# Performance work log

Hardware: AMD Instinct MI355X
Metric: run time of the kernel (lower is better)

The kernel has to match this reference:

```python
import jax, jax.numpy as jnp
import numpy as np

B, S, H = 4, 256, 128
EXP, DEPTH = 2, 2
MAX_LR = 0.01  # max_adaptive_lr


def l2n(x):
    # F.normalize(x, dim=-1), eps=1e-12
    return x / jnp.maximum(jnp.linalg.norm(x, axis=-1, keepdims=True), 1e-12)


def mem_apply(p, x):
    # ResLinear: depth residual MLP blocks (assumed; ResLinear not in snippet)
    h = x
    for (w1, b1, w2, b2) in p:
        h = h + jax.nn.silu(h @ w1 + b1) @ w2 + b2
    return h


def setup_inputs() -> dict:
    key = jax.random.key(0)
    ks = jax.random.split(key, 16)
    s = 0.02
    d = {
        'x': jax.random.normal(ks[0], (B, S, H), jnp.float32),
        'Wq': jax.random.normal(ks[1], (H, H), jnp.float32) * s,
        'Wk': jax.random.normal(ks[2], (H, H), jnp.float32) * s,
        'Wv': jax.random.normal(ks[3], (H, H), jnp.float32) * s,
        'w_lr': jax.random.normal(ks[4], (H, 1), jnp.float32) * s,
        'b_lr': jnp.zeros((1,), jnp.float32),
        'w_fg': jax.random.normal(ks[5], (H, 1), jnp.float32) * s,
        'b_fg': jnp.zeros((1,), jnp.float32),
        'w_mo': jax.random.normal(ks[6], (H, 1), jnp.float32) * s,
        'b_mo': jnp.zeros((1,), jnp.float32),
    }
    for i in range(DEPTH):
        d[f'w1_{i}'] = jax.random.normal(ks[7 + 2 * i], (H, H * EXP), jnp.float32) * s
        d[f'b1_{i}'] = jnp.zeros((H * EXP,), jnp.float32)
        d[f'w2_{i}'] = jax.random.normal(ks[8 + 2 * i], (H * EXP, H), jnp.float32) * s
        d[f'b2_{i}'] = jnp.zeros((H,), jnp.float32)
        d[f'm_w1_{i}'] = jnp.zeros((H, H * EXP), jnp.float32)
        d[f'm_b1_{i}'] = jnp.zeros((H * EXP,), jnp.float32)
        d[f'm_w2_{i}'] = jnp.zeros((H * EXP, H), jnp.float32)
        d[f'm_b2_{i}'] = jnp.zeros((H,), jnp.float32)
    return d


def _forward(x, Wq, Wk, Wv, w_lr, b_lr, w_fg, b_fg, w_mo, b_mo, p0, m0):
    q = l2n(jax.nn.silu(x @ Wq))                       # [B,S,H]
    k = l2n(jax.nn.silu(x @ Wk))
    v = jax.nn.silu(x @ Wv)
    theta = jax.nn.sigmoid(x @ w_lr + b_lr) * MAX_LR   # [B,S,1]
    alpha = jax.nn.sigmoid(x @ w_fg + b_fg)
    eta = jax.nn.sigmoid(x @ w_mo + b_mo)

    # per-batch copies of memory-net params / momentum
    pb = jax.tree.map(lambda a: jnp.broadcast_to(a, (B,) + a.shape), p0)
    mb = jax.tree.map(lambda a: jnp.broadcast_to(a, (B,) + a.shape), m0)

    def bc(s_, ref):  # [B,1] -> [B,1,...,1] to broadcast over batched param
        return s_.reshape((B,) + (1,) * (ref.ndim - 1))

    def loss_fn(p, k1, v1):
        pred = mem_apply(p, k1)            # [H]
        return jnp.mean((pred - v1) ** 2)  # mse.mean(-1).sum() for 1 token

    def step(carry, inp):
        cp, cm = carry
        kt, vt, qt, th, al, et = inp
        grads = jax.vmap(jax.grad(loss_fn))(cp, kt, vt)
        nm = jax.tree.map(lambda m, g: bc(et, m) * m - bc(th, m) * g, cm, grads)
        # NOTE: source decays the ORIGINAL params each step, not the carried ones
        npar = jax.tree.map(lambda p_, m: p_ * (1.0 - bc(al, m)) + m, pb, nm)
        out = jax.vmap(mem_apply, in_axes=(0, 0))(npar, qt)  # [B,H]
        new_carry = jax.tree.map(jax.lax.stop_gradient, (npar, nm))  # .detach()
        return new_carry, out

    tm = lambda a: jnp.swapaxes(a, 0, 1)  # time-major
    xs = (tm(k), tm(v), tm(q), tm(theta), tm(alpha), tm(eta))
    _, ys = jax.lax.scan(step, (pb, mb), xs)  # ys: [S,B,H]
    return jnp.swapaxes(ys, 0, 1)


def reference(x, Wq, Wk, Wv, w_lr, b_lr, w_fg, b_fg, w_mo, b_mo,
              w1_0, b1_0, w2_0, b2_0, w1_1, b1_1, w2_1, b2_1,
              m_w1_0, m_b1_0, m_w2_0, m_b2_0, m_w1_1, m_b1_1, m_w2_1, m_b2_1):
    p0 = ((w1_0, b1_0, w2_0, b2_0), (w1_1, b1_1, w2_1, b2_1))
    m0 = ((m_w1_0, m_b1_0, m_w2_0, m_b2_0), (m_w1_1, m_b1_1, m_w2_1, m_b2_1))
    return _forward(x, Wq, Wk, Wv, w_lr, b_lr, w_fg, b_fg, w_mo, b_mo, p0, m0)
```

## Files before the change

### kernel.cpp

```cpp
#include <hip/hip_runtime.h>


constexpr int HD  = 128;
constexpr int SEQ = 256;
constexpr int NB  = 4;
constexpr int ED  = 256;
constexpr int CW  = 64;
constexpr int NWG = 4;
constexpr int TOK = 8;

__device__ __forceinline__ float sigm(float x){
  float e;
  asm("v_exp_f32 %0, %1" : "=v"(e) : "v"(x * -1.44269504088896f));
  float r;
  asm("v_rcp_f32 %0, %1" : "=v"(r) : "v"(1.0f + e));
  return r;
}

template<int CTRL>
__device__ __forceinline__ float dpp_add(float x){
  int y = __builtin_amdgcn_update_dpp(0, __float_as_int(x), CTRL, 0xF, 0xF, true);
  return x + __int_as_float(y);
}
__device__ __forceinline__ float red32(float x){
  x = dpp_add<0xB1>(x);
  x = dpp_add<0x4E>(x);
  x = dpp_add<0x141>(x);
  x = dpp_add<0x140>(x);
  x += __int_as_float(__builtin_amdgcn_ds_swizzle(__float_as_int(x), 0x401F));
  return x;
}
__device__ __forceinline__ float red64(float x){
  x = red32(x);
  x += __shfl_xor(x, 32, 64);
  return x;
}

__global__ __launch_bounds__(128) void qkv_kernel(
    const float* __restrict__ x,
    const float* __restrict__ Wq, const float* __restrict__ Wk, const float* __restrict__ Wv,
    const float* __restrict__ w_lr, const float* __restrict__ b_lr,
    const float* __restrict__ w_fg, const float* __restrict__ b_fg,
    const float* __restrict__ w_mo, const float* __restrict__ b_mo,
    float* __restrict__ qb, float* __restrict__ kb, float* __restrict__ vb,
    float* __restrict__ thb, float* __restrict__ alb, float* __restrict__ etb)
{
  const int t0 = blockIdx.x * TOK;
  const int o  = threadIdx.x;
  __shared__ float xl[TOK][HD];
  __shared__ float red2[2][8];

  #pragma unroll
  for (int tt=0; tt<TOK; ++tt)
    xl[tt][o] = x[(size_t)(t0+tt)*HD + o];
  const float wl = w_lr[o], wf = w_fg[o], wm = w_mo[o];
  const float blr = b_lr[0], bfg = b_fg[0], bmo = b_mo[0];
  __syncthreads();

  float aq[TOK], ak[TOK], av[TOK];
  #pragma unroll
  for (int tt=0; tt<TOK; ++tt){ aq[tt]=0.f; ak[tt]=0.f; av[tt]=0.f; }
  for (int i=0; i<HD; i+=4){
    float wq0=Wq[(i+0)*HD+o], wk0=Wk[(i+0)*HD+o], wv0=Wv[(i+0)*HD+o];
    float wq1=Wq[(i+1)*HD+o], wk1=Wk[(i+1)*HD+o], wv1=Wv[(i+1)*HD+o];
    float wq2=Wq[(i+2)*HD+o], wk2=Wk[(i+2)*HD+o], wv2=Wv[(i+2)*HD+o];
    float wq3=Wq[(i+3)*HD+o], wk3=Wk[(i+3)*HD+o], wv3=Wv[(i+3)*HD+o];
    #pragma unroll
    for (int tt=0; tt<TOK; ++tt){
      float4 xv = *reinterpret_cast<const float4*>(&xl[tt][i]);
      aq[tt]=fmaf(xv.x,wq0,aq[tt]); ak[tt]=fmaf(xv.x,wk0,ak[tt]); av[tt]=fmaf(xv.x,wv0,av[tt]);
      aq[tt]=fmaf(xv.y,wq1,aq[tt]); ak[tt]=fmaf(xv.y,wk1,ak[tt]); av[tt]=fmaf(xv.y,wv1,av[tt]);
      aq[tt]=fmaf(xv.z,wq2,aq[tt]); ak[tt]=fmaf(xv.z,wk2,ak[tt]); av[tt]=fmaf(xv.z,wv2,av[tt]);
      aq[tt]=fmaf(xv.w,wq3,aq[tt]); ak[tt]=fmaf(xv.w,wk3,ak[tt]); av[tt]=fmaf(xv.w,wv3,av[tt]);
    }
  }
  #pragma unroll
  for (int tt=0; tt<TOK; ++tt){
    const size_t idx = (size_t)(t0+tt);
    float a_q=aq[tt], a_k=ak[tt], a_v=av[tt];
    float sq_ = a_q*sigm(a_q);
    float sk_ = a_k*sigm(a_k);
    float sv_ = a_v*sigm(a_v);
    float xo = xl[tt][o];
    float p0 = red64(sq_*sq_);
    float p1 = red64(sk_*sk_);
    float p2 = red64(xo*wl);
    float p3 = red64(xo*wf);
    float p4 = red64(xo*wm);
    if ((o&63)==0){
      int w = o>>6;
      red2[w][0]=p0; red2[w][1]=p1; red2[w][2]=p2; red2[w][3]=p3; red2[w][4]=p4;
    }
    __syncthreads();
    float nq = red2[0][0]+red2[1][0];
    float nk = red2[0][1]+red2[1][1];
    qb[idx*HD+o] = sq_ / fmaxf(sqrtf(nq), 1e-12f);
    kb[idx*HD+o] = sk_ / fmaxf(sqrtf(nk), 1e-12f);
    vb[idx*HD+o] = sv_;
    if (o==0){
      float dl = red2[0][2]+red2[1][2];
      float df = red2[0][3]+red2[1][3];
      float dm = red2[0][4]+red2[1][4];
      thb[idx] = sigm(dl + blr) * 0.01f;
      alb[idx] = sigm(df + bfg);
      etb[idx] = sigm(dm + bmo);
    }
    __syncthreads();
  }
}

__global__ __launch_bounds__(512, 1) void scan_kernel(
    const float* __restrict__ w1_0g, const float* __restrict__ b1_0g,
    const float* __restrict__ w2_0g, const float* __restrict__ b2_0g,
    const float* __restrict__ mw1_0g, const float* __restrict__ mb1_0g,
    const float* __restrict__ mw2_0g, const float* __restrict__ mb2_0g,
    const float* __restrict__ w1_1g, const float* __restrict__ b1_1g,
    const float* __restrict__ w2_1g, const float* __restrict__ b2_1g,
    const float* __restrict__ mw1_1g, const float* __restrict__ mb1_1g,
    const float* __restrict__ mw2_1g, const float* __restrict__ mb2_1g,
    const float* __restrict__ qbuf, const float* __restrict__ kbuf, const float* __restrict__ vbuf,
    const float* __restrict__ thb, const float* __restrict__ alb, const float* __restrict__ etb,
    unsigned long long* __restrict__ red, float* __restrict__ out)
{
  const int rb  = blockIdx.x;
  const int b   = rb & 7;
  if (b >= NB) return;
  const int wg  = rb >> 3;
  const int tid = threadIdx.x;
  const int iG  = tid & 31;
  const int jG  = tid >> 5;
  const int i0  = iG*4;
  const int j0  = jG*4;
  const int c0  = wg*CW;

  __shared__ float pw1L[2][16][512];
  __shared__ float pw2L[2][16][512];
  __shared__ float h1k[HD], h1q[HD], h2k[HD], gh1[HD];
  __shared__ float redbuf[8][256];
  __shared__ float b1p[2][CW], b1n[2][CW], b2p[2][32], b2n[2][32];

  float nw1[2][16], nw2[2][16];
  {
    const float* w1s[2]  = {w1_0g,  w1_1g};
    const float* mw1s[2] = {mw1_0g, mw1_1g};
    const float* w2s[2]  = {w2_0g,  w2_1g};
    const float* mw2s[2] = {mw2_0g, mw2_1g};
    #pragma unroll
    for (int l=0;l<2;l++){
      #pragma unroll
      for (int jj=0;jj<4;jj++){
        #pragma unroll
        for (int ii=0;ii<4;ii++){
          int gi1 = (i0+ii)*ED + (c0+j0+jj);
          float p1 = w1s[l][gi1];
          pw1L[l][jj*4+ii][tid] = p1;
          nw1[l][jj*4+ii] = p1 + mw1s[l][gi1];
          int gi2 = (c0+j0+jj)*HD + (i0+ii);
          float p2 = w2s[l][gi2];
          pw2L[l][jj*4+ii][tid] = p2;
          nw2[l][jj*4+ii] = p2 + mw2s[l][gi2];
        }
      }
    }
  }
  if (tid < CW){
    float p0a = b1_0g[c0+tid], p1a = b1_1g[c0+tid];
    b1p[0][tid] = p0a; b1n[0][tid] = p0a + mb1_0g[c0+tid];
    b1p[1][tid] = p1a; b1n[1][tid] = p1a + mb1_1g[c0+tid];
  } else if (tid < CW+32){
    int oo = tid - CW;
    float p0a = b2_0g[wg*32+oo], p1a = b2_1g[wg*32+oo];
    b2p[0][oo] = p0a; b2n[0][oo] = p0a + mb2_0g[wg*32+oo];
    b2p[1][oo] = p1a; b2n[1][oo] = p1a + mb2_1g[wg*32+oo];
  }

  auto pubstore = [&](int type, unsigned seq, int idx, float val){
    unsigned long long* p = red + (((b*3+type)*NWG + wg)*256 + idx);
    unsigned long long pk = ((unsigned long long)seq << 32) |
                            (unsigned long long)__float_as_uint(val);
    __hip_atomic_store(p, pk, __ATOMIC_RELAXED, __HIP_MEMORY_SCOPE_AGENT);
  };
  auto pollacc = [&](int type, unsigned seq, int idx, float own)->float{
    unsigned long long* base = red + ((b*3+type)*NWG)*256;
    const int wA=((wg+1)&3)*256+idx, wB=((wg+2)&3)*256+idx, wC=((wg+3)&3)*256+idx;
    unsigned long long vA = __hip_atomic_load(base+wA, __ATOMIC_RELAXED, __HIP_MEMORY_SCOPE_AGENT);
    unsigned long long vB = __hip_atomic_load(base+wB, __ATOMIC_RELAXED, __HIP_MEMORY_SCOPE_AGENT);
    unsigned long long vC = __hip_atomic_load(base+wC, __ATOMIC_RELAXED, __HIP_MEMORY_SCOPE_AGENT);
    float s = own; unsigned got = 0;
    while (got != 7u){
      if (!(got&1u)){
        if ((unsigned)(vA>>32)==seq){ s += __uint_as_float((unsigned)vA); got|=1u; }
        else vA = __hip_atomic_load(base+wA, __ATOMIC_RELAXED, __HIP_MEMORY_SCOPE_AGENT);
      }
      if (!(got&2u)){
        if ((unsigned)(vB>>32)==seq){ s += __uint_as_float((unsigned)vB); got|=2u; }
        else vB = __hip_atomic_load(base+wB, __ATOMIC_RELAXED, __HIP_MEMORY_SCOPE_AGENT);
      }
      if (!(got&4u)){
        if ((unsigned)(vC>>32)==seq){ s += __uint_as_float((unsigned)vC); got|=4u; }
        else vC = __hip_atomic_load(base+wC, __ATOMIC_RELAXED, __HIP_MEMORY_SCOPE_AGENT);
      }
    }
    return s;
  };

  float u1_r[4], s1_r[4], sg1_r[4], u2_r[4], s2_r[4], sg2_r[4], h1k_r[4], v_r[4], vc_r = 0.f;
  float kprev4[4];

  auto fwdFromU = [&](int t, bool writeOut, unsigned seq,
                      const float* uq, const float* uk, float ro){
    float sq1q[4];
    #pragma unroll
    for (int jj=0;jj<4;jj++){
      float vq = uq[jj], vk = uk[jj];
      u1_r[jj]=vk;
      float sgk = sigm(vk);
      sg1_r[jj]=sgk; s1_r[jj]=vk*sgk;
      sq1q[jj]=vq*sigm(vq);
    }
    float oq[4]={0,0,0,0}, ok[4]={0,0,0,0};
    #pragma unroll
    for (int jj=0;jj<4;jj++){
      #pragma unroll
      for (int oo=0;oo<4;oo++){
        float w = nw2[0][jj*4+oo];
        oq[oo] = fmaf(sq1q[jj], w, oq[oo]);
        ok[oo] = fmaf(s1_r[jj], w, ok[oo]);
      }
    }
    #pragma unroll
    for (int oo=0;oo<4;oo++){
      oq[oo] += __shfl_xor(oq[oo], 32, 64);
      ok[oo] += __shfl_xor(ok[oo], 32, 64);
    }
    if (!(tid & 32)){
      int wv = tid>>6;
      #pragma unroll
      for (int oo=0;oo<4;oo++){
        redbuf[wv][i0+oo]     = oq[oo];
        redbuf[wv][128+i0+oo] = ok[oo];
      }
    }
    __syncthreads();
    if (tid < 256){
      float p=0.f;
      #pragma unroll
      for (int w_=0; w_<8; w_++) p += redbuf[w_][tid];
      int o = tid & 127;
      if (o >= wg*32 && o < wg*32+32)
        p += b2n[0][o-wg*32];
      pubstore(1, seq, tid, p);
      float s0 = ro + pollacc(1, seq, tid, p);
      if (tid<128) h1q[o]=s0; else h1k[o]=s0;
    }
    __syncthreads();
    float aq2[4]={0,0,0,0}, ak2[4]={0,0,0,0};
    #pragma unroll
    for (int ii=0;ii<4;ii++){
      float qi = h1q[i0+ii], ki = h1k[i0+ii];
      h1k_r[ii] = ki;
      #pragma unroll
      for (int jj=0;jj<4;jj++){
        float w = nw1[1][jj*4+ii];
        aq2[jj] = fmaf(qi, w, aq2[jj]);
        ak2[jj] = fmaf(ki, w, ak2[jj]);
      }
    }
    #pragma unroll
    for (int jj=0;jj<4;jj++){
      aq2[jj] = red32(aq2[jj]);
      ak2[jj] = red32(ak2[jj]);
    }
    float sq2q[4];
    #pragma unroll
    for (int jj=0;jj<4;jj++){
      float bb = b1n[1][j0+jj];
      float vq = aq2[jj]+bb, vk = ak2[jj]+bb;
      u2_r[jj]=vk;
      float sgk = sigm(vk);
      sg2_r[jj]=sgk; s2_r[jj]=vk*sgk;
      sq2q[jj]=vq*sigm(vq);
    }
    #pragma unroll
    for (int oo=0;oo<4;oo++){ oq[oo]=0.f; ok[oo]=0.f; }
    #pragma unroll
    for (int jj=0;jj<4;jj++){
      #pragma unroll
      for (int oo=0;oo<4;oo++){
        float w = nw2[1][jj*4+oo];
        oq[oo] = fmaf(sq2q[jj], w, oq[oo]);
        ok[oo] = fmaf(s2_r[jj], w, ok[oo]);
      }
    }
    #pragma unroll
    for (int oo=0;oo<4;oo++){
      oq[oo] += __shfl_xor(oq[oo], 32, 64);
      ok[oo] += __shfl_xor(ok[oo], 32, 64);
    }
    if (!(tid & 32)){
      int wv = tid>>6;
      #pragma unroll
      for (int oo=0;oo<4;oo++){
        redbuf[wv][i0+oo]     = oq[oo];
        redbuf[wv][128+i0+oo] = ok[oo];
      }
    }
    __syncthreads();
    if (tid < 256){
      float p=0.f;
      #pragma unroll
      for (int w_=0; w_<8; w_++) p += redbuf[w_][tid];
      int o = tid & 127;
      if (o >= wg*32 && o < wg*32+32)
        p += b2n[1][o-wg*32];
      pubstore(2, seq, tid, p);
      float s0 = ((tid<128) ? h1q[o] : h1k[o]) + pollacc(2, seq, tid, p);
      if (tid<128){
        if (writeOut && o >= wg*32 && o < wg*32+32)
          out[((size_t)(b*SEQ + t))*HD + o] = s0;
      } else {
        h2k[o] = s0;
      }
    }
  };

  {
    #pragma unroll
    for (int ii=0;ii<4;ii++){
      kprev4[ii] = kbuf[((size_t)b*SEQ + 0)*HD + i0+ii];
      v_r[ii]    = vbuf[((size_t)b*SEQ + 0)*HD + i0+ii];
    }
    if (tid < HD) vc_r = vbuf[((size_t)b*SEQ + 0)*HD + tid];
    float ro0 = 0.f;
    if (tid >= 128 && tid < 256)
      ro0 = kbuf[((size_t)b*SEQ + 0)*HD + (tid-128)];
    __syncthreads();
    float ak0[4]={0,0,0,0};
    #pragma unroll
    for (int ii=0;ii<4;ii++){
      float ki = kprev4[ii];
      #pragma unroll
      for (int jj=0;jj<4;jj++)
        ak0[jj] = fmaf(ki, nw1[0][jj*4+ii], ak0[jj]);
    }
    #pragma unroll
    for (int jj=0;jj<4;jj++) ak0[jj] = red32(ak0[jj]);
    float uq0[4], uk0[4];
    #pragma unroll
    for (int jj=0;jj<4;jj++){
      float bb = b1n[0][j0+jj];
      uq0[jj] = bb;
      uk0[jj] = ak0[jj] + bb;
    }
    fwdFromU(0, false, 1u, uq0, uk0, ro0);
  }

  float dPrev = 1.f;
  for (int t=0; t<SEQ; ++t){
    const int tn = (t < SEQ-1) ? t+1 : SEQ-1;
    float qv4[4], kv4[4];
    #pragma unroll
    for (int ii=0;ii<4;ii++){
      qv4[ii] = qbuf[((size_t)b*SEQ + t )*HD + i0+ii];
      kv4[ii] = kbuf[((size_t)b*SEQ + tn)*HD + i0+ii];
    }
    float ro = 0.f;
    if (tid < 128)      ro = qbuf[((size_t)b*SEQ + t )*HD + tid];
    else if (tid < 256) ro = kbuf[((size_t)b*SEQ + tn)*HD + (tid-128)];
    const float th = thb[b*SEQ+t];
    const float al = alb[b*SEQ+t];
    const float et = etb[b*SEQ+t];
    const float nth = -th;
    const float dcur = 1.f - al;
    const float cP = dcur - et*dPrev;
    __syncthreads();
    float g2v_r[4];
    #pragma unroll
    for (int ii=0;ii<4;ii++) g2v_r[ii] = 0.015625f*(h2k[i0+ii] - v_r[ii]);
    float acc[4]={0,0,0,0};
    #pragma unroll
    for (int oo=0;oo<4;oo++){
      float go = g2v_r[oo];
      #pragma unroll
      for (int jj=0;jj<4;jj++)
        acc[jj] = fmaf(go, nw2[1][jj*4+oo], acc[jj]);
    }
    #pragma unroll
    for (int jj=0;jj<4;jj++) acc[jj] = red32(acc[jj]);
    float gu2r[4];
    #pragma unroll
    for (int jj=0;jj<4;jj++){
      float u=u2_r[jj]; float sg=sg2_r[jj];
      gu2r[jj] = acc[jj]*sg*fmaf(u, 1.f-sg, 1.f);
    }
    float a2[4]={0,0,0,0};
    #pragma unroll
    for (int jj=0;jj<4;jj++){
      float gj = gu2r[jj];
      #pragma unroll
      for (int ii=0;ii<4;ii++)
        a2[ii] = fmaf(gj, nw1[1][jj*4+ii], a2[ii]);
    }
    #pragma unroll
    for (int ii=0;ii<4;ii++) a2[ii] += __shfl_xor(a2[ii], 32, 64);
    if (!(tid & 32)){
      int wv = tid>>6;
      #pragma unroll
      for (int ii=0;ii<4;ii++) redbuf[wv][i0+ii] = a2[ii];
    }
    __syncthreads();
    const unsigned seqB = (unsigned)(t+1);
    float pB = 0.f, g2vc = 0.f;
    if (tid < HD){
      #pragma unroll
      for (int w_=0;w_<8;w_++) pB += redbuf[w_][tid];
      pubstore(0, seqB, tid, pB);
      g2vc = 0.015625f*(h2k[tid] - vc_r);
    }
    {
      float tg2[4], tv2[4];
      #pragma unroll
      for (int jj=0;jj<4;jj++) tg2[jj] = nth*gu2r[jj];
      #pragma unroll
      for (int ii=0;ii<4;ii++) tv2[ii] = nth*g2v_r[ii];
      #pragma unroll
      for (int jj=0;jj<4;jj++){
        float g2jt = tg2[jj], s2j = s2_r[jj];
        #pragma unroll
        for (int ii=0;ii<4;ii++){
          int e = jj*4+ii;
          nw1[1][e] = fmaf(et, nw1[1][e],
                           fmaf(cP, pw1L[1][e][tid], h1k_r[ii]*g2jt));
          nw2[1][e] = fmaf(et, nw2[1][e],
                           fmaf(cP, pw2L[1][e][tid], s2j*tv2[ii]));
        }
      }
      if (iG==0){
        #pragma unroll
        for (int jj=0;jj<4;jj++)
          b1n[1][j0+jj] = fmaf(et, b1n[1][j0+jj],
                               fmaf(cP, b1p[1][j0+jj], tg2[jj]));
      }
      if (jG==0 && iG>=wg*8 && iG<wg*8+8){
        #pragma unroll
        for (int ii=0;ii<4;ii++)
          b2n[1][i0+ii-wg*32] = fmaf(et, b2n[1][i0+ii-wg*32],
                                     fmaf(cP, b2p[1][i0+ii-wg*32], tv2[ii]));
      }
    }
    #pragma unroll
    for (int ii=0;ii<4;ii++)
      v_r[ii] = vbuf[((size_t)b*SEQ + tn)*HD + i0+ii];
    if (tid < HD) vc_r = vbuf[((size_t)b*SEQ + tn)*HD + tid];
    if (tid < HD)
      gh1[tid] = g2vc + pollacc(0, seqB, tid, pB);
    __syncthreads();
    float gh1_r[4];
    #pragma unroll
    for (int ii=0;ii<4;ii++) gh1_r[ii] = gh1[i0+ii];
    #pragma unroll
    for (int jj=0;jj<4;jj++) acc[jj]=0.f;
    #pragma unroll
    for (int oo=0;oo<4;oo++){
      float go = gh1_r[oo];
      #pragma unroll
      for (int jj=0;jj<4;jj++)
        acc[jj] = fmaf(go, nw2[0][jj*4+oo], acc[jj]);
    }
    #pragma unroll
    for (int jj=0;jj<4;jj++) acc[jj] = red32(acc[jj]);
    float gu1r[4];
    #pragma unroll
    for (int jj=0;jj<4;jj++){
      float u=u1_r[jj]; float sg=sg1_r[jj];
      gu1r[jj] = acc[jj]*sg*fmaf(u, 1.f-sg, 1.f);
    }
    {
      float tg1[4], tv0[4];
      #pragma unroll
      for (int jj=0;jj<4;jj++) tg1[jj] = nth*gu1r[jj];
      #pragma unroll
      for (int ii=0;ii<4;ii++) tv0[ii] = nth*gh1_r[ii];
      #pragma unroll
      for (int jj=0;jj<4;jj++){
        float g1jt = tg1[jj], s1j = s1_r[jj];
        #pragma unroll
        for (int ii=0;ii<4;ii++){
          int e = jj*4+ii;
          nw1[0][e] = fmaf(et, nw1[0][e],
                           fmaf(cP, pw1L[0][e][tid], kprev4[ii]*g1jt));
          nw2[0][e] = fmaf(et, nw2[0][e],
                           fmaf(cP, pw2L[0][e][tid], s1j*tv0[ii]));
        }
      }
      if (iG==0){
        #pragma unroll
        for (int jj=0;jj<4;jj++)
          b1n[0][j0+jj] = fmaf(et, b1n[0][j0+jj],
                               fmaf(cP, b1p[0][j0+jj], tg1[jj]));
      }
      if (jG==0 && iG>=wg*8 && iG<wg*8+8){
        #pragma unroll
        for (int ii=0;ii<4;ii++)
          b2n[0][i0+ii-wg*32] = fmaf(et, b2n[0][i0+ii-wg*32],
                                     fmaf(cP, b2p[0][i0+ii-wg*32], tv0[ii]));
      }
    }
    float aq[4]={0,0,0,0}, ak[4]={0,0,0,0};
    #pragma unroll
    for (int ii=0;ii<4;ii++){
      float qi = qv4[ii], ki = kv4[ii];
      #pragma unroll
      for (int jj=0;jj<4;jj++){
        float w = nw1[0][jj*4+ii];
        aq[jj] = fmaf(qi, w, aq[jj]);
        ak[jj] = fmaf(ki, w, ak[jj]);
      }
    }
    #pragma unroll
    for (int jj=0;jj<4;jj++){
      aq[jj] = red32(aq[jj]);
      ak[jj] = red32(ak[jj]);
    }
    float uqf[4], ukf[4];
    #pragma unroll
    for (int jj=0;jj<4;jj++){
      float bb = b1n[0][j0+jj];
      uqf[jj] = aq[jj] + bb;
      ukf[jj] = ak[jj] + bb;
    }
    #pragma unroll
    for (int ii=0;ii<4;ii++) kprev4[ii] = kv4[ii];
    dPrev = dcur;
    fwdFromU(t, true, (unsigned)(t+2), uqf, ukf, ro);
  }
}

extern "C" void kernel_launch(void* const* d_in, const int* in_sizes, int n_in,
                              void* d_out, int out_size, void* d_ws, size_t ws_size,
                              hipStream_t stream)
{
  (void)in_sizes; (void)n_in; (void)out_size; (void)ws_size;
  const float* x    = (const float*)d_in[0];
  const float* Wq   = (const float*)d_in[1];
  const float* Wk   = (const float*)d_in[2];
  const float* Wv   = (const float*)d_in[3];
  const float* w_lr = (const float*)d_in[4];
  const float* b_lr = (const float*)d_in[5];
  const float* w_fg = (const float*)d_in[6];
  const float* b_fg = (const float*)d_in[7];
  const float* w_mo = (const float*)d_in[8];
  const float* b_mo = (const float*)d_in[9];
  const float* w1_0 = (const float*)d_in[10];
  const float* b1_0 = (const float*)d_in[11];
  const float* w2_0 = (const float*)d_in[12];
  const float* b2_0 = (const float*)d_in[13];
  const float* m_w1_0 = (const float*)d_in[14];
  const float* m_b1_0 = (const float*)d_in[15];
  const float* m_w2_0 = (const float*)d_in[16];
  const float* m_b2_0 = (const float*)d_in[17];
  const float* w1_1 = (const float*)d_in[18];
  const float* b1_1 = (const float*)d_in[19];
  const float* w2_1 = (const float*)d_in[20];
  const float* b2_1 = (const float*)d_in[21];
  const float* m_w1_1 = (const float*)d_in[22];
  const float* m_b1_1 = (const float*)d_in[23];
  const float* m_w2_1 = (const float*)d_in[24];
  const float* m_b2_1 = (const float*)d_in[25];

  float* wsf = (float*)d_ws;
  unsigned long long* red = (unsigned long long*)d_ws;
  float* qbuf = wsf + 32768;
  float* kbuf = qbuf + NB*SEQ*HD;
  float* vbuf = kbuf + NB*SEQ*HD;
  float* thb  = vbuf + NB*SEQ*HD;
  float* alb  = thb + NB*SEQ;
  float* etb  = alb + NB*SEQ;

  qkv_kernel<<<dim3(NB*SEQ/TOK), dim3(HD), 0, stream>>>(
      x, Wq, Wk, Wv, w_lr, b_lr, w_fg, b_fg, w_mo, b_mo,
      qbuf, kbuf, vbuf, thb, alb, etb);

  scan_kernel<<<dim3(4*NWG*2), dim3(512), 0, stream>>>(
      w1_0, b1_0, w2_0, b2_0, m_w1_0, m_b1_0, m_w2_0, m_b2_0,
      w1_1, b1_1, w2_1, b2_1, m_w1_1, m_b1_1, m_w2_1, m_b2_1,
      qbuf, kbuf, vbuf, thb, alb, etb,
      red, (float*)d_out);
}
```

Measured before the change: 1.786 ms.

## Publish per-wave partials to global slots and reduce all-to-all without block barriers

Replaces the intra-block LDS reduction, the __syncthreads before it, and the single per-workgroup published partial with direct per-wave atomic publishes to global slots. Consumers sum 16 wave partials using vectorized uncached loads, with half the threads pre-summing two source workgroups and handing the result over through LDS flags. Every workgroup now keeps full copies of the b2 biases, so bias updates are replicated rather than owned by one slice. The aim is to remove barrier and serialization latency on the sequential scan's critical path, at the cost of more global traffic, spin-waits on LDS flags, and a larger workspace.

```diff
diff --git a/kernel.cpp b/kernel.cpp
--- a/kernel.cpp
+++ b/kernel.cpp
@@ -8,6 +8,10 @@
 constexpr int CW  = 64;
 constexpr int NWG = 4;
 constexpr int TOK = 8;
+constexpr int BATSLOT = 20480;
+
+typedef unsigned long long ull;
+typedef unsigned int v4u __attribute__((ext_vector_type(4)));
 
 __device__ __forceinline__ float sigm(float x){
   float e;
@@ -34,6 +38,43 @@
   x = red32(x);
   x += __shfl_xor(x, 32, 64);
   return x;
+}
+
+__device__ __forceinline__ float sum16(const ull* a, const ull* b, unsigned seq){
+  v4u r0,r1,r2,r3,r4,r5,r6,r7;
+  asm volatile(
+    "global_load_dwordx4 %0, %8, off sc0 sc1\n\t"
+    "global_load_dwordx4 %1, %9, off sc0 sc1\n\t"
+    "global_load_dwordx4 %2, %10, off sc0 sc1\n\t"
+    "global_load_dwordx4 %3, %11, off sc0 sc1\n\t"
+    "global_load_dwordx4 %4, %12, off sc0 sc1\n\t"
+    "global_load_dwordx4 %5, %13, off sc0 sc1\n\t"
+    "global_load_dwordx4 %6, %14, off sc0 sc1\n\t"
+    "global_load_dwordx4 %7, %15, off sc0 sc1\n\t"
+    "s_waitcnt vmcnt(0)"
+    : "=&v"(r0),"=&v"(r1),"=&v"(r2),"=&v"(r3),
+      "=&v"(r4),"=&v"(r5),"=&v"(r6),"=&v"(r7)
+    : "v"(a),"v"(a+2),"v"(a+4),"v"(a+6),
+      "v"(b),"v"(b+2),"v"(b+4),"v"(b+6)
+    : "memory");
+  float s = 0.f; unsigned got = 0;
+  v4u rr[8] = {r0,r1,r2,r3,r4,r5,r6,r7};
+  #pragma unroll
+  for (int i=0;i<8;i++){
+    if (rr[i].y==seq){ s += __uint_as_float(rr[i].x); got |= 1u<<(2*i); }
+    if (rr[i].w==seq){ s += __uint_as_float(rr[i].z); got |= 1u<<(2*i+1); }
+  }
+  while (got != 0xFFFFu){
+    #pragma unroll
+    for (int i=0;i<16;i++){
+      if (!(got & (1u<<i))){
+        const ull* p = (i<8) ? (a+i) : (b+(i-8));
+        ull v = __hip_atomic_load(p, __ATOMIC_RELAXED, __HIP_MEMORY_SCOPE_AGENT);
+        if ((unsigned)(v>>32)==seq){ s += __uint_as_float((unsigned)v); got |= 1u<<i; }
+      }
+    }
+  }
+  return s;
 }
 
 __global__ __launch_bounds__(128) void qkv_kernel(
@@ -120,7 +161,7 @@
     const float* __restrict__ mw2_1g, const float* __restrict__ mb2_1g,
     const float* __restrict__ qbuf, const float* __restrict__ kbuf, const float* __restrict__ vbuf,
     const float* __restrict__ thb, const float* __restrict__ alb, const float* __restrict__ etb,
-    unsigned long long* __restrict__ red, float* __restrict__ out)
+    ull* __restrict__ red, float* __restrict__ out)
 {
   const int rb  = blockIdx.x;
   const int b   = rb & 7;
@@ -132,12 +173,19 @@
   const int i0  = iG*4;
   const int j0  = jG*4;
   const int c0  = wg*CW;
+  const int wv  = tid >> 6;
+
+  ull* SB = red + (size_t)b*BATSLOT;
+  auto sB = [&](int w_,int pos){ return SB + (((w_<<7)+pos)<<3); };
+  auto s1 = [&](int w_,int pos){ return SB + 4096  + (((w_<<8)+pos)<<3); };
+  auto s2 = [&](int w_,int pos){ return SB + 12288 + (((w_<<8)+pos)<<3); };
 
   __shared__ float pw1L[2][16][512];
   __shared__ float pw2L[2][16][512];
   __shared__ float h1k[HD], h1q[HD], h2k[HD], gh1[HD];
-  __shared__ float redbuf[8][256];
-  __shared__ float b1p[2][CW], b1n[2][CW], b2p[2][32], b2n[2][32];
+  __shared__ float b1p[2][CW], b1n[2][CW];
+  __shared__ float b2p0f[HD], b2n0f[HD], b2p1f[HD], b2n1f[HD];
+  __shared__ unsigned pcT1[256], pcV1[256], pcT2[256], pcV2[256], pcTB[128], pcVB[128];
 
   float nw1[2][16], nw2[2][16];
   {
@@ -167,48 +215,29 @@
     float p0a = b1_0g[c0+tid], p1a = b1_1g[c0+tid];
     b1p[0][tid] = p0a; b1n[0][tid] = p0a + mb1_0g[c0+tid];
     b1p[1][tid] = p1a; b1n[1][tid] = p1a + mb1_1g[c0+tid];
-  } else if (tid < CW+32){
-    int oo = tid - CW;
-    float p0a = b2_0g[wg*32+oo], p1a = b2_1g[wg*32+oo];
-    b2p[0][oo] = p0a; b2n[0][oo] = p0a + mb2_0g[wg*32+oo];
-    b2p[1][oo] = p1a; b2n[1][oo] = p1a + mb2_1g[wg*32+oo];
-  }
-
-  auto pubstore = [&](int type, unsigned seq, int idx, float val){
-    unsigned long long* p = red + (((b*3+type)*NWG + wg)*256 + idx);
-    unsigned long long pk = ((unsigned long long)seq << 32) |
-                            (unsigned long long)__float_as_uint(val);
-    __hip_atomic_store(p, pk, __ATOMIC_RELAXED, __HIP_MEMORY_SCOPE_AGENT);
+  }
+  if (tid < 128){
+    float pa0 = b2_0g[tid], pa1 = b2_1g[tid];
+    b2p0f[tid] = pa0; b2n0f[tid] = pa0 + mb2_0g[tid];
+    b2p1f[tid] = pa1; b2n1f[tid] = pa1 + mb2_1g[tid];
+    pcTB[tid] = 0;
+  }
+  if (tid < 256){ pcT1[tid] = 0; pcT2[tid] = 0; }
+
+  auto pub = [&](ull* slot, unsigned seq, float val){
+    __hip_atomic_store(slot, ((ull)seq<<32) | (ull)__float_as_uint(val),
+                       __ATOMIC_RELAXED, __HIP_MEMORY_SCOPE_AGENT);
   };
-  auto pollacc = [&](int type, unsigned seq, int idx, float own)->float{
-    unsigned long long* base = red + ((b*3+type)*NWG)*256;
-    const int wA=((wg+1)&3)*256+idx, wB=((wg+2)&3)*256+idx, wC=((wg+3)&3)*256+idx;
-    unsigned long long vA = __hip_atomic_load(base+wA, __ATOMIC_RELAXED, __HIP_MEMORY_SCOPE_AGENT);
-    unsigned long long vB = __hip_atomic_load(base+wB, __ATOMIC_RELAXED, __HIP_MEMORY_SCOPE_AGENT);
-    unsigned long long vC = __hip_atomic_load(base+wC, __ATOMIC_RELAXED, __HIP_MEMORY_SCOPE_AGENT);
-    float s = own; unsigned got = 0;
-    while (got != 7u){
-      if (!(got&1u)){
-        if ((unsigned)(vA>>32)==seq){ s += __uint_as_float((unsigned)vA); got|=1u; }
-        else vA = __hip_atomic_load(base+wA, __ATOMIC_RELAXED, __HIP_MEMORY_SCOPE_AGENT);
-      }
-      if (!(got&2u)){
-        if ((unsigned)(vB>>32)==seq){ s += __uint_as_float((unsigned)vB); got|=2u; }
-        else vB = __hip_atomic_load(base+wB, __ATOMIC_RELAXED, __HIP_MEMORY_SCOPE_AGENT);
-      }
-      if (!(got&4u)){
-        if ((unsigned)(vC>>32)==seq){ s += __uint_as_float((unsigned)vC); got|=4u; }
-        else vC = __hip_atomic_load(base+wC, __ATOMIC_RELAXED, __HIP_MEMORY_SCOPE_AGENT);
-      }
-    }
-    return s;
-  };
+
+  volatile unsigned* vT1 = pcT1; volatile unsigned* vV1 = pcV1;
+  volatile unsigned* vT2 = pcT2; volatile unsigned* vV2 = pcV2;
+  volatile unsigned* vTB = pcTB; volatile unsigned* vVB = pcVB;
 
   float u1_r[4], s1_r[4], sg1_r[4], u2_r[4], s2_r[4], sg2_r[4], h1k_r[4], v_r[4], vc_r = 0.f;
   float kprev4[4];
 
-  auto fwdFromU = [&](int t, bool writeOut, unsigned seq,
-                      const float* uq, const float* uk, float ro){
+  auto fwd = [&](int t, bool writeOut, unsigned seq,
+                 const float* uq, const float* uk, float ro){
     float sq1q[4];
     #pragma unroll
     for (int jj=0;jj<4;jj++){
@@ -234,24 +263,23 @@
       ok[oo] += __shfl_xor(ok[oo], 32, 64);
     }
     if (!(tid & 32)){
-      int wv = tid>>6;
       #pragma unroll
       for (int oo=0;oo<4;oo++){
-        redbuf[wv][i0+oo]     = oq[oo];
-        redbuf[wv][128+i0+oo] = ok[oo];
-      }
-    }
-    __syncthreads();
+        pub(s1(wg, i0+oo)     + wv, seq, oq[oo]);
+        pub(s1(wg, 128+i0+oo) + wv, seq, ok[oo]);
+      }
+    }
     if (tid < 256){
-      float p=0.f;
-      #pragma unroll
-      for (int w_=0; w_<8; w_++) p += redbuf[w_][tid];
-      int o = tid & 127;
-      if (o >= wg*32 && o < wg*32+32)
-        p += b2n[0][o-wg*32];
-      pubstore(1, seq, tid, p);
-      float s0 = ro + pollacc(1, seq, tid, p);
-      if (tid<128) h1q[o]=s0; else h1k[o]=s0;
+      const int p = tid, o = p & 127;
+      float sA = sum16(s1((wg+1)&3, p), s1((wg+2)&3, p), seq);
+      while (vT1[p] != seq) {}
+      float tot = sA + __uint_as_float(vV1[p]) + b2n0f[o] + ro;
+      if (p < 128) h1q[o] = tot; else h1k[o] = tot;
+    } else {
+      const int p = tid - 256;
+      float sP = sum16(s1((wg+3)&3, p), s1(wg, p), seq);
+      vV1[p] = __float_as_uint(sP);
+      vT1[p] = seq;
     }
     __syncthreads();
     float aq2[4]={0,0,0,0}, ak2[4]={0,0,0,0};
@@ -298,29 +326,29 @@
       ok[oo] += __shfl_xor(ok[oo], 32, 64);
     }
     if (!(tid & 32)){
-      int wv = tid>>6;
       #pragma unroll
       for (int oo=0;oo<4;oo++){
-        redbuf[wv][i0+oo]     = oq[oo];
-        redbuf[wv][128+i0+oo] = ok[oo];
-      }
-    }
-    __syncthreads();
-    if (tid < 256){
-      float p=0.f;
-      #pragma unroll
-      for (int w_=0; w_<8; w_++) p += redbuf[w_][tid];
-      int o = tid & 127;
-      if (o >= wg*32 && o < wg*32+32)
-        p += b2n[1][o-wg*32];
-      pubstore(2, seq, tid, p);
-      float s0 = ((tid<128) ? h1q[o] : h1k[o]) + pollacc(2, seq, tid, p);
-      if (tid<128){
-        if (writeOut && o >= wg*32 && o < wg*32+32)
-          out[((size_t)(b*SEQ + t))*HD + o] = s0;
-      } else {
-        h2k[o] = s0;
-      }
+        pub(s2(wg, i0+oo)     + wv, seq, oq[oo]);
+        pub(s2(wg, 128+i0+oo) + wv, seq, ok[oo]);
+      }
+    }
+    if (tid < 128){
+      const int o = tid;
+      float sA = sum16(s2((wg+1)&3, o), s2((wg+2)&3, o), seq);
+      while (vT2[o] != seq) {}
+      float tot = h1q[o] + sA + __uint_as_float(vV2[o]) + b2n1f[o];
+      if (writeOut && (o>>5)==wg)
+        out[((size_t)(b*SEQ + t))*HD + o] = tot;
+    } else if (tid < 256){
+      const int o = tid-128, p = tid;
+      float sA = sum16(s2((wg+1)&3, p), s2((wg+2)&3, p), seq);
+      while (vT2[p] != seq) {}
+      h2k[o] = h1k[o] + sA + __uint_as_float(vV2[p]) + b2n1f[o];
+    } else {
+      const int p = tid - 256;
+      float sP = sum16(s2((wg+3)&3, p), s2(wg, p), seq);
+      vV2[p] = __float_as_uint(sP);
+      vT2[p] = seq;
     }
   };
 
@@ -352,12 +380,13 @@
       uq0[jj] = bb;
       uk0[jj] = ak0[jj] + bb;
     }
-    fwdFromU(0, false, 1u, uq0, uk0, ro0);
+    fwd(0, false, 1u, uq0, uk0, ro0);
   }
 
   float dPrev = 1.f;
   for (int t=0; t<SEQ; ++t){
     const int tn = (t < SEQ-1) ? t+1 : SEQ-1;
+    __syncthreads();
     float qv4[4], kv4[4];
     #pragma unroll
     for (int ii=0;ii<4;ii++){
@@ -373,7 +402,6 @@
     const float nth = -th;
     const float dcur = 1.f - al;
     const float cP = dcur - et*dPrev;
-    __syncthreads();
     float g2v_r[4];
     #pragma unroll
     for (int ii=0;ii<4;ii++) g2v_r[ii] = 0.015625f*(h2k[i0+ii] - v_r[ii]);
@@ -403,20 +431,14 @@
     }
     #pragma unroll
     for (int ii=0;ii<4;ii++) a2[ii] += __shfl_xor(a2[ii], 32, 64);
+    const unsigned seqB = (unsigned)(t+1);
     if (!(tid & 32)){
-      int wv = tid>>6;
-      #pragma unroll
-      for (int ii=0;ii<4;ii++) redbuf[wv][i0+ii] = a2[ii];
-    }
-    __syncthreads();
-    const unsigned seqB = (unsigned)(t+1);
-    float pB = 0.f, g2vc = 0.f;
-    if (tid < HD){
-      #pragma unroll
-      for (int w_=0;w_<8;w_++) pB += redbuf[w_][tid];
-      pubstore(0, seqB, tid, pB);
-      g2vc = 0.015625f*(h2k[tid] - vc_r);
-    }
+      #pragma unroll
+      for (int ii=0;ii<4;ii++)
+        pub(sB(wg, i0+ii) + wv, seqB, a2[ii]);
+    }
+    float g2vc = 0.f;
+    if (tid < 128) g2vc = 0.015625f*(h2k[tid] - vc_r);
     {
       float tg2[4], tv2[4];
       #pragma unroll
@@ -441,19 +463,25 @@
           b1n[1][j0+jj] = fmaf(et, b1n[1][j0+jj],
                                fmaf(cP, b1p[1][j0+jj], tg2[jj]));
       }
-      if (jG==0 && iG>=wg*8 && iG<wg*8+8){
-        #pragma unroll
-        for (int ii=0;ii<4;ii++)
-          b2n[1][i0+ii-wg*32] = fmaf(et, b2n[1][i0+ii-wg*32],
-                                     fmaf(cP, b2p[1][i0+ii-wg*32], tv2[ii]));
-      }
+      if (tid < 128)
+        b2n1f[tid] = fmaf(et, b2n1f[tid], fmaf(cP, b2p1f[tid], nth*g2vc));
     }
     #pragma unroll
     for (int ii=0;ii<4;ii++)
       v_r[ii] = vbuf[((size_t)b*SEQ + tn)*HD + i0+ii];
     if (tid < HD) vc_r = vbuf[((size_t)b*SEQ + tn)*HD + tid];
-    if (tid < HD)
-      gh1[tid] = g2vc + pollacc(0, seqB, tid, pB);
+    if (tid < 128){
+      float sA = sum16(sB((wg+1)&3, tid), sB((wg+2)&3, tid), seqB);
+      while (vTB[tid] != seqB) {}
+      float tot = g2vc + sA + __uint_as_float(vVB[tid]);
+      gh1[tid] = tot;
+      b2n0f[tid] = fmaf(et, b2n0f[tid], fmaf(cP, b2p0f[tid], nth*tot));
+    } else if (tid < 256){
+      const int p = tid - 128;
+      float sP = sum16(sB((wg+3)&3, p), sB(wg, p), seqB);
+      vVB[p] = __float_as_uint(sP);
+      vTB[p] = seqB;
+    }
     __syncthreads();
     float gh1_r[4];
     #pragma unroll
@@ -499,12 +527,6 @@
           b1n[0][j0+jj] = fmaf(et, b1n[0][j0+jj],
                                fmaf(cP, b1p[0][j0+jj], tg1[jj]));
       }
-      if (jG==0 && iG>=wg*8 && iG<wg*8+8){
-        #pragma unroll
-        for (int ii=0;ii<4;ii++)
-          b2n[0][i0+ii-wg*32] = fmaf(et, b2n[0][i0+ii-wg*32],
-                                     fmaf(cP, b2p[0][i0+ii-wg*32], tv0[ii]));
-      }
     }
     float aq[4]={0,0,0,0}, ak[4]={0,0,0,0};
     #pragma unroll
@@ -532,7 +554,7 @@
     #pragma unroll
     for (int ii=0;ii<4;ii++) kprev4[ii] = kv4[ii];
     dPrev = dcur;
-    fwdFromU(t, true, (unsigned)(t+2), uqf, ukf, ro);
+    fwd(t, true, (unsigned)(t+2), uqf, ukf, ro);
   }
 }
 
@@ -569,8 +591,8 @@
   const float* m_b2_1 = (const float*)d_in[25];
 
   float* wsf = (float*)d_ws;
-  unsigned long long* red = (unsigned long long*)d_ws;
-  float* qbuf = wsf + 32768;
+  ull* red = (ull*)d_ws;
+  float* qbuf = wsf + 163840;
   float* kbuf = qbuf + NB*SEQ*HD;
   float* vbuf = kbuf + NB*SEQ*HD;
   float* thb  = vbuf + NB*SEQ*HD;
```

Result: slower. 6.723 ms (+276.5%).
